# Kernel tuning notes

Measured on AMD Instinct MI355X. Metric: run time of the kernel, lower is better.

The kernel has to match this reference:

```python
import jax, jax.numpy as jnp
import numpy as np


def recursive_fht(x):
    # Faithful vectorized version of the module's recursive butterfly FHT
    # (twiddle = cas(2*pi*n/N), no flipped-odd term, exactly as in the source).
    N = x.shape[-1]
    if N == 1:
        return x
    e = recursive_fht(x[..., ::2])
    o = recursive_fht(x[..., 1::2])
    n = jnp.arange(N // 2, dtype=x.dtype)
    t = jnp.cos(2 * jnp.pi * n / N) + jnp.sin(2 * jnp.pi * n / N)
    return jnp.concatenate([e + t * o, e - t * o], axis=-1)


def compl_mul1d(x1, x2):
    # x1: [B, i, modes], x2: [i, o, modes]; flips along axis 0 as in the source
    x1f = x1[::-1]
    x2f = x2[::-1]
    return 0.5 * (jnp.einsum('bix,iox->box', x1, x2)
                  - jnp.einsum('bix,iox->box', x1f, x2f)
                  + jnp.einsum('bix,iox->box', x1, x2f)
                  + jnp.einsum('bix,iox->box', x1f, x2))


def idht(X):
    # Inverse discrete Hartley transform via the cas matrix (DHT is an
    # involution up to 1/K). K = N//2+1 is not a power of 2, so a dense
    # transform is used. Compute-bound batched GEMM.
    K = X.shape[-1]
    n = jnp.arange(K, dtype=X.dtype)
    ang = 2.0 * jnp.pi * jnp.outer(n, n) / K
    cas = jnp.cos(ang) + jnp.sin(ang)  # [K, K]
    return jnp.einsum('bck,kn->bcn', X, cas) / K


def setup_inputs() -> dict:
    key = jax.random.key(0)
    k1, k2 = jax.random.split(key)
    B, Cin, Cout, N, modes1 = 32, 64, 64, 4096, 1024
    x = jax.random.normal(k1, (B, Cin, N), dtype=jnp.float32)
    scale = 1.0 / (Cin * Cout)
    weights1 = scale * jax.random.uniform(k2, (Cin, Cout, modes1), dtype=jnp.float32)
    return {"x": x, "weights1": weights1, "modes1": modes1}


def reference(x, weights1, modes1):
    B, C, N = x.shape
    # dht with threshold=1.0: FHT along last axis, low-pass filter is a no-op
    x_ht = recursive_fht(x)
    K = N // 2 + 1
    out_ht = jnp.zeros((B, C, K), dtype=x.dtype)
    out_ht = out_ht.at[:, :, :modes1].set(compl_mul1d(x_ht[:, :, :modes1], weights1))
    return idht(out_ht)  # [B, C, N//2+1]
```

## Files before the change

### kernel.cpp

```cpp
#include <hip/hip_runtime.h>
#include <hip/hip_bf16.h>

#define BATCH 32
#define CIN   64
#define COUT  64
#define NFFT  4096
#define MODES 1024
#define KOUT  2049
#define NPAD  2112

typedef __bf16 bf16x8 __attribute__((ext_vector_type(8)));
typedef float  f32x4  __attribute__((ext_vector_type(4)));

#define AS1 __attribute__((address_space(1)))
#define AS3 __attribute__((address_space(3)))

static __device__ __forceinline__ void gl_lds16(const void* g, void* l) {
    __builtin_amdgcn_global_load_lds((const AS1 void*)g, (AS3 void*)l, 16, 0, 0);
}

static __device__ __forceinline__ void bfly4(float eA, float eB, float oA, float oB,
                                             float t, float c0, float c1,
                                             float& w0, float& w1, float& w2, float& w3) {
    float PA = fmaf(t, oA, eA), MA = fmaf(-t, oA, eA);
    float PB = fmaf(t, oB, eB), MB = fmaf(-t, oB, eB);
    w0 = fmaf(c0, PB, PA);
    w2 = fmaf(-c0, PB, PA);
    w1 = fmaf(c1, MB, MA);
    w3 = fmaf(-c1, MB, MA);
}

#define NCHUNK ((NPAD / 16) * (MODES / 32) * 64)

__global__ void fill_tables(float* __restrict__ tw, __hip_bfloat16* __restrict__ c2f) {
    int gid = blockIdx.x * 256 + threadIdx.x;
    if (gid < NCHUNK) {
        int nl  = gid & 15;
        int kc  = (gid >> 4) & 3;
        int blk = gid >> 6;
        int kb  = blk & 31;
        int gn  = blk >> 5;
        int n = gn * 16 + nl;
        int kbase = kb * 32 + kc * 8;
        unsigned short v8[8];
        if (n < KOUT) {
#pragma unroll
            for (int j = 0; j < 8; ++j) {
                int k = kbase + j;
                int m = (k * n) % KOUT;
                float ang = 6.28318530717958647692f * (float)m / (float)KOUT;
                float v = (cosf(ang) + sinf(ang)) * (1.0f / (float)KOUT);
                __hip_bfloat16 h = __float2bfloat16(v);
                v8[j] = *(unsigned short*)&h;
            }
        } else {
#pragma unroll
            for (int j = 0; j < 8; ++j) v8[j] = 0;
        }
        *(ushort4*)((char*)c2f + (size_t)gid * 16)     = make_ushort4(v8[0], v8[1], v8[2], v8[3]);
        *(ushort4*)((char*)c2f + (size_t)gid * 16 + 8) = make_ushort4(v8[4], v8[5], v8[6], v8[7]);
    } else {
        int t = gid - NCHUNK;
        if (t < NFFT) {
            if (t == 0) { tw[0] = 1.0f; return; }
            int h = 1 << (31 - __clz(t));
            int n = t - h;
            float ang = 3.14159265358979323846f * (float)n / (float)h;
            tw[t] = cosf(ang) + sinf(ang);
        }
    }
}

__global__ __launch_bounds__(256) void fht_kernel(const float* __restrict__ x,
                                                  const float* __restrict__ tw,
                                                  float* __restrict__ xh) {
    __shared__ float ldsA[4352];
    __shared__ float ldsB[4352];
    const int t = threadIdx.x;
    const int row = blockIdx.x;
    const float* xr = x + (size_t)row * NFFT;

    float r[4][4];
#pragma unroll
    for (int a = 0; a < 4; ++a)
#pragma unroll
        for (int c = 0; c < 4; ++c)
            r[a][c] = xr[t + 256 * a + 1024 * c];

    float o1[4][4];
#pragma unroll
    for (int a = 0; a < 4; ++a) {
        float PA = r[a][0] + r[a][2], MA = r[a][0] - r[a][2];
        float PB = r[a][1] + r[a][3], MB = r[a][1] - r[a][3];
        o1[a][0] = PA + PB;
        o1[a][2] = PA - PB;
        o1[a][1] = MA + MB;
        o1[a][3] = MA - MB;
    }
    float o2[4][4];
#pragma unroll
    for (int kap = 0; kap < 4; ++kap) {
        float tt = tw[4 + kap], c0 = tw[8 + kap], c1 = tw[12 + kap];
        bfly4(o1[0][kap], o1[1][kap], o1[2][kap], o1[3][kap], tt, c0, c1,
              o2[kap][0], o2[kap][1], o2[kap][2], o2[kap][3]);
    }
#pragma unroll
    for (int kap = 0; kap < 4; ++kap)
#pragma unroll
        for (int c = 0; c < 4; ++c) {
            int p = t + 256 * kap + 1024 * c;
            ldsA[p + (p >> 4)] = o2[kap][c];
        }
    __syncthreads();

    const int kap2 = t >> 4, gp = t & 15;
    float r2[4][4];
#pragma unroll
    for (int a = 0; a < 4; ++a)
#pragma unroll
        for (int c = 0; c < 4; ++c) {
            int p = 256 * kap2 + gp + 16 * a + 64 * c;
            r2[a][c] = ldsA[p + (p >> 4)];
        }
    float o3[4][4];
    {
        float tt = tw[16 + kap2], c0 = tw[32 + kap2], c1 = tw[48 + kap2];
#pragma unroll
        for (int a = 0; a < 4; ++a)
            bfly4(r2[a][0], r2[a][1], r2[a][2], r2[a][3], tt, c0, c1,
                  o3[a][0], o3[a][1], o3[a][2], o3[a][3]);
    }
    float o4[4][4];
#pragma unroll
    for (int c = 0; c < 4; ++c) {
        int kap3 = kap2 + 16 * c;
        float tt = tw[64 + kap3], c0 = tw[128 + kap3], c1 = tw[192 + kap3];
        bfly4(o3[0][c], o3[1][c], o3[2][c], o3[3][c], tt, c0, c1,
              o4[c][0], o4[c][1], o4[c][2], o4[c][3]);
    }
#pragma unroll
    for (int c = 0; c < 4; ++c)
#pragma unroll
        for (int cc = 0; cc < 4; ++cc) {
            int p = t + 256 * c + 1024 * cc;
            ldsB[p + (p >> 4)] = o4[c][cc];
        }
    __syncthreads();

    float r3[4][4];
#pragma unroll
    for (int g = 0; g < 4; ++g)
#pragma unroll
        for (int c = 0; c < 4; ++c) {
            int p = 16 * t + g + 4 * c;
            r3[g][c] = ldsB[p + (p >> 4)];
        }
    float o5[4][4];
    {
        float tt = tw[256 + t], c0 = tw[512 + t], c1 = tw[768 + t];
#pragma unroll
        for (int g = 0; g < 4; ++g)
            bfly4(r3[g][0], r3[g][1], r3[g][2], r3[g][3], tt, c0, c1,
                  o5[g][0], o5[g][1], o5[g][2], o5[g][3]);
    }
    float* xo = xh + (size_t)row * MODES;
#pragma unroll
    for (int c = 0; c < 4; ++c) {
        float tt = tw[1024 + t + 256 * c];
        float c0 = tw[2048 + t + 256 * c];
        float PA = fmaf(tt, o5[2][c], o5[0][c]);
        float PB = fmaf(tt, o5[3][c], o5[1][c]);
        xo[t + 256 * c] = fmaf(c0, PB, PA);
    }
}

__global__ __launch_bounds__(256) void mix_kernel(const f32x4* __restrict__ xh,
                                                  const f32x4* __restrict__ w,
                                                  ushort4* __restrict__ y_hi) {
    const int kl = threadIdx.x & 63;
    const int jg = threadIdx.x >> 6;
    const int k4 = blockIdx.x * 64 + kl;
    const int b  = blockIdx.y;
    const int rb = (BATCH - 1) - b;
    const int o  = blockIdx.z * 4 + jg;

    f32x4 accb = (f32x4){0.f, 0.f, 0.f, 0.f};
    f32x4 accr = (f32x4){0.f, 0.f, 0.f, 0.f};

#pragma unroll 4
    for (int i = 0; i < 32; ++i) {
        const int mi = 63 - i;
        f32x4 xai = xh[(size_t)(b  * CIN + i ) * 256 + k4];
        f32x4 xam = xh[(size_t)(b  * CIN + mi) * 256 + k4];
        f32x4 xbi = xh[(size_t)(rb * CIN + i ) * 256 + k4];
        f32x4 xbm = xh[(size_t)(rb * CIN + mi) * 256 + k4];
        f32x4 w1 = w[(size_t)(i  * COUT + o) * 256 + k4];
        f32x4 w2 = w[(size_t)(mi * COUT + o) * 256 + k4];
        f32x4 sa = xai + xam;
        f32x4 da = xai - xam;
        f32x4 sb = xbi + xbm;
        f32x4 db = xbi - xbm;
        f32x4 wp = w1 + w2, wm = w1 - w2;
        accb += sa * wp + db * wm;
        accr += sb * wp + da * wm;
    }

    const size_t ib = (size_t)(b  * COUT + o) * 256 + k4;
    const size_t ir = (size_t)(rb * COUT + o) * 256 + k4;
    f32x4 vb = accb * 0.5f;
    f32x4 vr = accr * 0.5f;
    __hip_bfloat16 b0 = __float2bfloat16(vb.x), b1 = __float2bfloat16(vb.y),
                   b2 = __float2bfloat16(vb.z), b3 = __float2bfloat16(vb.w);
    __hip_bfloat16 r0 = __float2bfloat16(vr.x), r1 = __float2bfloat16(vr.y),
                   r2 = __float2bfloat16(vr.z), r3 = __float2bfloat16(vr.w);
    y_hi[ib] = make_ushort4(*(unsigned short*)&b0, *(unsigned short*)&b1,
                            *(unsigned short*)&b2, *(unsigned short*)&b3);
    y_hi[ir] = make_ushort4(*(unsigned short*)&r0, *(unsigned short*)&r1,
                            *(unsigned short*)&r2, *(unsigned short*)&r3);
}

__global__ __launch_bounds__(128) void idht_mfma(const __hip_bfloat16* __restrict__ yh,
                                                 const __hip_bfloat16* __restrict__ c2f,
                                                 float* __restrict__ out) {
    __shared__ __align__(16) char sa[2][4 * 1024];

    const int tid  = threadIdx.x;
    const int lane = tid & 63;
    const int wave = tid >> 6;
    const int rbase = blockIdx.x * 64;
    const int gn0   = blockIdx.y * 4;
    const int nbase = gn0 * 16;

    const int lrow = (lane & 15) * 2048;
    const int lchk = (lane >> 4) * 16;

    const char* ga = (const char*)yh + (size_t)rbase * 2048;
    const char* gb = (const char*)c2f;

    f32x4 acc[2][4];
#pragma unroll
    for (int mt = 0; mt < 2; ++mt)
#pragma unroll
        for (int nt = 0; nt < 4; ++nt) acc[mt][nt] = (f32x4){0.f, 0.f, 0.f, 0.f};

    auto stageA = [&](int bi, int k0) {
#pragma unroll
        for (int r = 0; r < 2; ++r) {
            int g = wave * 2 + r;
            gl_lds16(ga + (size_t)(g * 16) * 2048 + lrow + lchk + k0 * 2,
                     sa[bi] + g * 1024);
        }
    };
    auto loadB = [&](int ks, bf16x8* b_) {
#pragma unroll
        for (int nt = 0; nt < 4; ++nt) {
            size_t ch = ((size_t)(gn0 + nt) * 32 + ks) * 64 + lane;
            b_[nt] = *(const bf16x8*)(gb + ch * 16);
        }
    };

    stageA(0, 0);
    bf16x8 bcur[4];
    loadB(0, bcur);
    int cur = 0;
    for (int ks = 0; ks < MODES / 32; ++ks) {
        __syncthreads();
        if (ks + 1 < MODES / 32) stageA(cur ^ 1, (ks + 1) * 32);
        bf16x8 bnext[4];
        int kn = (ks + 1 < MODES / 32) ? ks + 1 : ks;
        loadB(kn, bnext);
        bf16x8 a_[2];
#pragma unroll
        for (int mt = 0; mt < 2; ++mt)
            a_[mt] = *(const bf16x8*)(sa[cur] + (wave * 2 + mt) * 1024 + lane * 16);
#pragma unroll
        for (int mt = 0; mt < 2; ++mt)
#pragma unroll
            for (int nt = 0; nt < 4; ++nt)
                acc[mt][nt] = __builtin_amdgcn_mfma_f32_16x16x32_bf16(a_[mt], bcur[nt], acc[mt][nt], 0, 0, 0);
#pragma unroll
        for (int nt = 0; nt < 4; ++nt) bcur[nt] = bnext[nt];
        cur ^= 1;
    }

#pragma unroll
    for (int mt = 0; mt < 2; ++mt) {
        int row = rbase + wave * 32 + mt * 16 + (lane >> 4) * 4;
#pragma unroll
        for (int nt = 0; nt < 4; ++nt) {
            int col = nbase + nt * 16 + (lane & 15);
            if (col < KOUT) {
#pragma unroll
                for (int r = 0; r < 4; ++r)
                    out[(size_t)(row + r) * KOUT + col] = acc[mt][nt][r];
            }
        }
    }
}

extern "C" void kernel_launch(void* const* d_in, const int* in_sizes, int n_in,
                              void* d_out, int out_size, void* d_ws, size_t ws_size,
                              hipStream_t stream) {
    const float* x = (const float*)d_in[0];
    const float* w = (const float*)d_in[1];
    float* out = (float*)d_out;

    float* tw = (float*)d_ws;
    float* xh = tw + NFFT;
    __hip_bfloat16* y_hi = (__hip_bfloat16*)(xh + (size_t)BATCH * CIN * MODES);
    __hip_bfloat16* c2f  = y_hi + (size_t)BATCH * COUT * MODES;

    fill_tables<<<(NCHUNK + NFFT + 255) / 256, 256, 0, stream>>>(tw, c2f);
    fht_kernel<<<BATCH * CIN, 256, 0, stream>>>(x, tw, xh);
    mix_kernel<<<dim3(4, 16, 16), 256, 0, stream>>>((const f32x4*)xh, (const f32x4*)w,
                                                    (ushort4*)y_hi);
    idht_mfma<<<dim3((BATCH * COUT) / 64, NPAD / 64), 128, 0, stream>>>(y_hi, c2f, out);
}
```

Measured before the change: 154.0 us.

## Store FHT output in bf16 and remap mix kernel thread layout

The FHT intermediate is now written as bf16 instead of fp32, halving its write and read traffic between the FHT and mode-mixing kernels. The mix kernel is restructured: each thread handles 8 modes, 512-thread blocks group 32 output channels and 8 batch pairs, and loads are 16-byte bf16x8 and float4 vectors. Adjacent threads now differ mainly in output channel, so activation loads are shared across the block through cache. This adds bf16 rounding error on the transform output before the weight multiply.

```diff
diff --git a/kernel.cpp b/kernel.cpp
--- a/kernel.cpp
+++ b/kernel.cpp
@@ -17,6 +17,29 @@
 
 static __device__ __forceinline__ void gl_lds16(const void* g, void* l) {
     __builtin_amdgcn_global_load_lds((const AS1 void*)g, (AS3 void*)l, 16, 0, 0);
+}
+
+static __device__ __forceinline__ float bf2f(unsigned short s) {
+    return __uint_as_float(((unsigned)s) << 16);
+}
+static __device__ __forceinline__ void cvt8(bf16x8 v, f32x4& lo, f32x4& hi) {
+    union { bf16x8 b; unsigned short s[8]; } u;
+    u.b = v;
+    lo = (f32x4){bf2f(u.s[0]), bf2f(u.s[1]), bf2f(u.s[2]), bf2f(u.s[3])};
+    hi = (f32x4){bf2f(u.s[4]), bf2f(u.s[5]), bf2f(u.s[6]), bf2f(u.s[7])};
+}
+static __device__ __forceinline__ bf16x8 pack8(f32x4 lo, f32x4 hi) {
+    union { bf16x8 b; unsigned short s[8]; } u;
+    __hip_bfloat16 h;
+    h = __float2bfloat16(lo.x); u.s[0] = *(unsigned short*)&h;
+    h = __float2bfloat16(lo.y); u.s[1] = *(unsigned short*)&h;
+    h = __float2bfloat16(lo.z); u.s[2] = *(unsigned short*)&h;
+    h = __float2bfloat16(lo.w); u.s[3] = *(unsigned short*)&h;
+    h = __float2bfloat16(hi.x); u.s[4] = *(unsigned short*)&h;
+    h = __float2bfloat16(hi.y); u.s[5] = *(unsigned short*)&h;
+    h = __float2bfloat16(hi.z); u.s[6] = *(unsigned short*)&h;
+    h = __float2bfloat16(hi.w); u.s[7] = *(unsigned short*)&h;
+    return u.b;
 }
 
 static __device__ __forceinline__ void bfly4(float eA, float eB, float oA, float oB,
@@ -73,7 +96,7 @@
 
 __global__ __launch_bounds__(256) void fht_kernel(const float* __restrict__ x,
                                                   const float* __restrict__ tw,
-                                                  float* __restrict__ xh) {
+                                                  __hip_bfloat16* __restrict__ xh) {
     __shared__ float ldsA[4352];
     __shared__ float ldsB[4352];
     const int t = threadIdx.x;
@@ -163,60 +186,71 @@
             bfly4(r3[g][0], r3[g][1], r3[g][2], r3[g][3], tt, c0, c1,
                   o5[g][0], o5[g][1], o5[g][2], o5[g][3]);
     }
-    float* xo = xh + (size_t)row * MODES;
+    __hip_bfloat16* xo = xh + (size_t)row * MODES;
 #pragma unroll
     for (int c = 0; c < 4; ++c) {
         float tt = tw[1024 + t + 256 * c];
         float c0 = tw[2048 + t + 256 * c];
         float PA = fmaf(tt, o5[2][c], o5[0][c]);
         float PB = fmaf(tt, o5[3][c], o5[1][c]);
-        xo[t + 256 * c] = fmaf(c0, PB, PA);
-    }
-}
-
-__global__ __launch_bounds__(256) void mix_kernel(const f32x4* __restrict__ xh,
-                                                  const f32x4* __restrict__ w,
-                                                  ushort4* __restrict__ y_hi) {
-    const int kl = threadIdx.x & 63;
-    const int jg = threadIdx.x >> 6;
-    const int k4 = blockIdx.x * 64 + kl;
-    const int b  = blockIdx.y;
-    const int rb = (BATCH - 1) - b;
-    const int o  = blockIdx.z * 4 + jg;
-
-    f32x4 accb = (f32x4){0.f, 0.f, 0.f, 0.f};
-    f32x4 accr = (f32x4){0.f, 0.f, 0.f, 0.f};
+        xo[t + 256 * c] = __float2bfloat16(fmaf(c0, PB, PA));
+    }
+}
+
+__global__ __launch_bounds__(512) void mix_kernel(const __hip_bfloat16* __restrict__ xh,
+                                                  const float* __restrict__ w,
+                                                  __hip_bfloat16* __restrict__ y) {
+    const int tid = threadIdx.x;
+    const int kl  = tid & 1;
+    const int og  = (tid >> 1) & 31;
+    const int bpl = tid >> 6;
+    const int bp  = blockIdx.y * 8 + bpl;
+    const int rb  = (BATCH - 1) - bp;
+    const int o   = blockIdx.z * 32 + og;
+    const int k8  = blockIdx.x * 2 + kl;
+
+    f32x4 accb0 = {0,0,0,0}, accb1 = {0,0,0,0};
+    f32x4 accr0 = {0,0,0,0}, accr1 = {0,0,0,0};
+
+    const __hip_bfloat16* xb  = xh + (size_t)(bp * CIN) * MODES + k8 * 8;
+    const __hip_bfloat16* xrb = xh + (size_t)(rb * CIN) * MODES + k8 * 8;
+    const float* wo = w + (size_t)o * MODES + k8 * 8;
 
 #pragma unroll 4
     for (int i = 0; i < 32; ++i) {
         const int mi = 63 - i;
-        f32x4 xai = xh[(size_t)(b  * CIN + i ) * 256 + k4];
-        f32x4 xam = xh[(size_t)(b  * CIN + mi) * 256 + k4];
-        f32x4 xbi = xh[(size_t)(rb * CIN + i ) * 256 + k4];
-        f32x4 xbm = xh[(size_t)(rb * CIN + mi) * 256 + k4];
-        f32x4 w1 = w[(size_t)(i  * COUT + o) * 256 + k4];
-        f32x4 w2 = w[(size_t)(mi * COUT + o) * 256 + k4];
-        f32x4 sa = xai + xam;
-        f32x4 da = xai - xam;
-        f32x4 sb = xbi + xbm;
-        f32x4 db = xbi - xbm;
-        f32x4 wp = w1 + w2, wm = w1 - w2;
-        accb += sa * wp + db * wm;
-        accr += sb * wp + da * wm;
-    }
-
-    const size_t ib = (size_t)(b  * COUT + o) * 256 + k4;
-    const size_t ir = (size_t)(rb * COUT + o) * 256 + k4;
-    f32x4 vb = accb * 0.5f;
-    f32x4 vr = accr * 0.5f;
-    __hip_bfloat16 b0 = __float2bfloat16(vb.x), b1 = __float2bfloat16(vb.y),
-                   b2 = __float2bfloat16(vb.z), b3 = __float2bfloat16(vb.w);
-    __hip_bfloat16 r0 = __float2bfloat16(vr.x), r1 = __float2bfloat16(vr.y),
-                   r2 = __float2bfloat16(vr.z), r3 = __float2bfloat16(vr.w);
-    y_hi[ib] = make_ushort4(*(unsigned short*)&b0, *(unsigned short*)&b1,
-                            *(unsigned short*)&b2, *(unsigned short*)&b3);
-    y_hi[ir] = make_ushort4(*(unsigned short*)&r0, *(unsigned short*)&r1,
-                            *(unsigned short*)&r2, *(unsigned short*)&r3);
+        bf16x8 xai = *(const bf16x8*)(xb  + (size_t)i  * MODES);
+        bf16x8 xam = *(const bf16x8*)(xb  + (size_t)mi * MODES);
+        bf16x8 xbi = *(const bf16x8*)(xrb + (size_t)i  * MODES);
+        bf16x8 xbm = *(const bf16x8*)(xrb + (size_t)mi * MODES);
+        f32x4 w1a = *(const f32x4*)(wo + (size_t)(i  * COUT) * MODES);
+        f32x4 w1b = *(const f32x4*)(wo + (size_t)(i  * COUT) * MODES + 4);
+        f32x4 w2a = *(const f32x4*)(wo + (size_t)(mi * COUT) * MODES);
+        f32x4 w2b = *(const f32x4*)(wo + (size_t)(mi * COUT) * MODES + 4);
+
+        f32x4 ai_lo, ai_hi, am_lo, am_hi, bi_lo, bi_hi, bm_lo, bm_hi;
+        cvt8(xai, ai_lo, ai_hi);
+        cvt8(xam, am_lo, am_hi);
+        cvt8(xbi, bi_lo, bi_hi);
+        cvt8(xbm, bm_lo, bm_hi);
+
+        f32x4 sa0 = ai_lo + am_lo, sa1 = ai_hi + am_hi;
+        f32x4 da0 = ai_lo - am_lo, da1 = ai_hi - am_hi;
+        f32x4 sb0 = bi_lo + bm_lo, sb1 = bi_hi + bm_hi;
+        f32x4 db0 = bi_lo - bm_lo, db1 = bi_hi - bm_hi;
+        f32x4 wp0 = w1a + w2a, wm0 = w1a - w2a;
+        f32x4 wp1 = w1b + w2b, wm1 = w1b - w2b;
+
+        accb0 += sa0 * wp0 + db0 * wm0;
+        accb1 += sa1 * wp1 + db1 * wm1;
+        accr0 += sb0 * wp0 + da0 * wm0;
+        accr1 += sb1 * wp1 + da1 * wm1;
+    }
+
+    bf16x8 vb = pack8(accb0 * 0.5f, accb1 * 0.5f);
+    bf16x8 vr = pack8(accr0 * 0.5f, accr1 * 0.5f);
+    *(bf16x8*)(y + (size_t)(bp * COUT + o) * MODES + k8 * 8) = vb;
+    *(bf16x8*)(y + (size_t)(rb * COUT + o) * MODES + k8 * 8) = vr;
 }
 
 __global__ __launch_bounds__(128) void idht_mfma(const __hip_bfloat16* __restrict__ yh,
@@ -306,13 +340,12 @@
     float* out = (float*)d_out;
 
     float* tw = (float*)d_ws;
-    float* xh = tw + NFFT;
-    __hip_bfloat16* y_hi = (__hip_bfloat16*)(xh + (size_t)BATCH * CIN * MODES);
-    __hip_bfloat16* c2f  = y_hi + (size_t)BATCH * COUT * MODES;
+    __hip_bfloat16* xh  = (__hip_bfloat16*)(tw + NFFT);
+    __hip_bfloat16* y   = xh + (size_t)BATCH * CIN * MODES;
+    __hip_bfloat16* c2f = y + (size_t)BATCH * COUT * MODES;
 
     fill_tables<<<(NCHUNK + NFFT + 255) / 256, 256, 0, stream>>>(tw, c2f);
     fht_kernel<<<BATCH * CIN, 256, 0, stream>>>(x, tw, xh);
-    mix_kernel<<<dim3(4, 16, 16), 256, 0, stream>>>((const f32x4*)xh, (const f32x4*)w,
-                                                    (ushort4*)y_hi);
-    idht_mfma<<<dim3((BATCH * COUT) / 64, NPAD / 64), 128, 0, stream>>>(y_hi, c2f, out);
-}
+    mix_kernel<<<dim3(64, 2, 2), 512, 0, stream>>>(xh, w, y);
+    idht_mfma<<<dim3((BATCH * COUT) / 64, NPAD / 64), 128, 0, stream>>>(y, c2f, out);
+}
```

Measured after the change: 160.4 us. +4.2%, slower.
